# Kernel tuning notes

Measured on AMD Instinct MI355X. Metric: run time of the kernel, lower is better.

Reference implementation:

```python
import jax, jax.numpy as jnp
import numpy as np

N, FEAT, D, K, L, H, NCLS = 4096, 512, 64, 100, 3, 8, 2
EPS = 1e-15

def _ln(x, g, b, eps=1e-6):
    m = x.mean(-1, keepdims=True)
    v = x.var(-1, keepdims=True)
    return (x - m) * jax.lax.rsqrt(v + eps) * g + b


def setup_inputs():
    key = jax.random.key(0)
    ks = jax.random.split(key, 12)
    w = lambda k, shape: jax.random.normal(k, shape, jnp.float32) * 0.02
    return {
        "node_feat": jax.random.normal(ks[0], (1, N, FEAT), jnp.float32),
        "adj": jax.random.uniform(ks[1], (1, N, N), jnp.float32),
        "conv_w": w(ks[2], (FEAT, D)), "conv_b": jnp.zeros((D,), jnp.float32),
        "bn_g": jnp.ones((D,), jnp.float32), "bn_b": jnp.zeros((D,), jnp.float32),
        "pool_w": w(ks[3], (D, K)), "pool_b": jnp.zeros((K,), jnp.float32),
        "cls_token": jnp.zeros((1, 1, D), jnp.float32),
        "ln1_g": jnp.ones((L, D), jnp.float32), "ln1_b": jnp.zeros((L, D), jnp.float32),
        "qkv_w": w(ks[4], (L, D, 3 * D)), "qkv_b": jnp.zeros((L, 3 * D), jnp.float32),
        "proj_w": w(ks[5], (L, D, D)), "proj_b": jnp.zeros((L, D), jnp.float32),
        "ln2_g": jnp.ones((L, D), jnp.float32), "ln2_b": jnp.zeros((L, D), jnp.float32),
        "fc1_w": w(ks[6], (L, D, 4 * D)), "fc1_b": jnp.zeros((L, 4 * D), jnp.float32),
        "fc2_w": w(ks[7], (L, 4 * D, D)), "fc2_b": jnp.zeros((L, D), jnp.float32),
        "norm_g": jnp.ones((D,), jnp.float32), "norm_b": jnp.zeros((D,), jnp.float32),
        "head_w": w(ks[8], (D, NCLS)), "head_b": jnp.zeros((NCLS,), jnp.float32),
    }


def _forward(node_feat, adj, conv_w, conv_b, bn_g, bn_b, pool_w, pool_b, cls_token,
             ln1_g, ln1_b, qkv_w, qkv_b, proj_w, proj_b, ln2_g, ln2_b,
             fc1_w, fc1_b, fc2_w, fc2_b, norm_g, norm_b, head_w, head_b):
    x = node_feat  # mask is all ones -> X = mask*X is a no-op
    # --- GCNBlock: propagate + self loop + linear + BatchNorm(train stats) + L2 norm ---
    y = jnp.matmul(adj, x) + x                 # [1,N,F]
    y = y @ conv_w + conv_b                    # [1,N,D]
    m = y.mean(axis=(0, 1))
    v = y.var(axis=(0, 1))
    y = (y - m) * jax.lax.rsqrt(v + 1e-5) * bn_g + bn_b
    y = y / jnp.maximum(jnp.linalg.norm(y, axis=2, keepdims=True), 1e-12)
    # --- cluster assignment ---
    s = jax.nn.softmax(y @ pool_w + pool_b, axis=-1)   # [1,N,K]
    # --- dense_mincut_pool ---
    out = jnp.einsum('bnk,bnd->bkd', s, y)             # [1,K,D]
    sa = s[0].T @ adj[0]                               # [K,N] (the torch.sparse.mm)
    out_adj = (sa @ s[0])[None]                        # [1,K,K]
    mincut_num = jnp.trace(out_adj, axis1=1, axis2=2)  # [1]
    d_flat = adj.sum(-1)                               # [1,N] degrees
    # trace(S^T diag(d) S) = sum_i d_i * ||s_i||^2
    mincut_den = jnp.sum(d_flat[0] * jnp.sum(s[0] ** 2, axis=-1))[None]
    mincut_loss = jnp.mean(-(mincut_num / mincut_den))
    ss = jnp.einsum('bnk,bnl->bkl', s, s)
    i_s = jnp.eye(K, dtype=ss.dtype)
    ortho_loss = jnp.mean(jnp.linalg.norm(
        ss / jnp.linalg.norm(ss, axis=(-1, -2), keepdims=True) - i_s / jnp.linalg.norm(i_s),
        axis=(-1, -2)))
    ind = jnp.arange(K)
    out_adj = out_adj.at[:, ind, ind].set(0.0)
    dd = jnp.sqrt(out_adj.sum(-1))[:, None] + EPS      # [1,1,K]
    out_adj = out_adj / dd / jnp.swapaxes(dd, 1, 2)    # (returned by pool; unused downstream)
    # --- transformer over [cls] + K cluster tokens ---
    t = jnp.concatenate([jnp.broadcast_to(cls_token, (1, 1, D)), out], axis=1)  # [1,K+1,D]
    hd = D // H
    scale = hd ** -0.5
    for l in range(L):
        h = _ln(t, ln1_g[l], ln1_b[l])
        qkv = h @ qkv_w[l] + qkv_b[l]
        q, k, vv = jnp.split(qkv, 3, axis=-1)
        sp = lambda a: a.reshape(1, -1, H, hd).transpose(0, 2, 1, 3)
        q, k, vv = sp(q), sp(k), sp(vv)
        att = jax.nn.softmax(jnp.einsum('bhqd,bhkd->bhqk', q, k) * scale, axis=-1)
        o = jnp.einsum('bhqk,bhkd->bhqd', att, vv).transpose(0, 2, 1, 3).reshape(1, -1, D)
        t = t + (o @ proj_w[l] + proj_b[l])
        h = _ln(t, ln2_g[l], ln2_b[l])
        t = t + (jax.nn.gelu(h @ fc1_w[l] + fc1_b[l], approximate=False) @ fc2_w[l] + fc2_b[l])
    t = _ln(t, norm_g, norm_b)
    logits = t[:, 0] @ head_w + head_b                 # [1,NCLS]
    return logits, mincut_loss, ortho_loss


def reference(node_feat, adj, conv_w, conv_b, bn_g, bn_b, pool_w, pool_b, cls_token,
              ln1_g, ln1_b, qkv_w, qkv_b, proj_w, proj_b, ln2_g, ln2_b,
              fc1_w, fc1_b, fc2_w, fc2_b, norm_g, norm_b, head_w, head_b):
    return _forward(node_feat, adj, conv_w, conv_b, bn_g, bn_b, pool_w, pool_b, cls_token,
                    ln1_g, ln1_b, qkv_w, qkv_b, proj_w, proj_b, ln2_g, ln2_b,
                    fc1_w, fc1_b, fc2_w, fc2_b, norm_g, norm_b, head_w, head_b)
```

## Files before the change

kernel.cpp:

```cpp
#include <hip/hip_runtime.h>
#include <hip/hip_bf16.h>
#include <math.h>

#define NN   4096
#define FEAT 512
#define DIM  64
#define KC   100
#define LL   3

#define OFF_DFLAT   0
#define OFF_CHSUM   4096
#define OFF_CHSQ    4160
#define ZERO_FLOATS 4224
#define OFF_XW      4224
#define OFF_YPART   (OFF_XW + NN*DIM)
#define OFF_GPART   (OFF_YPART + 8*NN*DIM)
#define OFF_Y0      (OFF_GPART + 64*128*192)
#define OFF_TBUF    (OFF_Y0 + NN*DIM)
#define OFF_QKV     (OFF_TBUF + 101*DIM)
#define OFF_SS      (OFF_QKV + 101*192)
#define OFF_DENP    (OFF_SS + KC*KC)
#define OFF_NUMP    (OFF_DENP + 1024)
#define OFF_SB16    (OFF_NUMP + 1024)
#define OFF_STB16   (OFF_SB16 + NN*128/2)
#define OFF_YNT16   (OFF_STB16 + NN*128/2)
#define OFF_XWT16   (OFF_YNT16 + NN*DIM/2)

typedef __attribute__((ext_vector_type(8))) short bfrag;
typedef __attribute__((ext_vector_type(4))) float ffrag;

__device__ __forceinline__ unsigned short f2bf(float f) {
    union { float f; unsigned u; } v; v.f = f;
    return (unsigned short)((v.u + 0x7FFFu + ((v.u >> 16) & 1u)) >> 16);
}
__device__ __forceinline__ float bf2f(unsigned short u) {
    union { unsigned u; float f; } v; v.u = (unsigned)u << 16; return v.f;
}
__device__ __forceinline__ unsigned int pk2(float a, float b) {
    __hip_bfloat162 h = __float22bfloat162_rn(make_float2(a, b));
    return *(unsigned int*)&h;
}

__device__ __forceinline__ float wsum(float v) {
#pragma unroll
    for (int o = 32; o > 0; o >>= 1) v += __shfl_xor(v, o, 64);
    return v;
}
__device__ __forceinline__ float wmax(float v) {
#pragma unroll
    for (int o = 32; o > 0; o >>= 1) v = fmaxf(v, __shfl_xor(v, o, 64));
    return v;
}
__device__ __forceinline__ float hsum32(float v) {
#pragma unroll
    for (int o = 16; o > 0; o >>= 1) v += __shfl_xor(v, o, 64);
    return v;
}
__device__ __forceinline__ float hmax32(float v) {
#pragma unroll
    for (int o = 16; o > 0; o >>= 1) v = fmaxf(v, __shfl_xor(v, o, 64));
    return v;
}

__global__ __launch_bounds__(256) void xwk(const float* __restrict__ x,
                                           const float* __restrict__ B,
                                           float* __restrict__ xw,
                                           unsigned short* __restrict__ xwT,
                                           float* __restrict__ zws) {
    __shared__ float a_sh[16 * 68];
    __shared__ float b_sh[64 * 68];
    __shared__ unsigned short tl[64 * 17];
    const int t = threadIdx.x, rb = blockIdx.x;
    if (rb < 17) {
        const int zi = rb * 256 + t;
        if (zi < ZERO_FLOATS) zws[zi] = 0.f;
    }
    const int r = t >> 4, cg = (t & 15) * 4;
    float4 acc = make_float4(0.f, 0.f, 0.f, 0.f);
    for (int kt = 0; kt < FEAT; kt += 64) {
        *(float4*)&a_sh[(t >> 4) * 68 + (t & 15) * 4] =
            *(const float4*)(x + (size_t)(rb * 16 + (t >> 4)) * FEAT + kt + (t & 15) * 4);
#pragma unroll
        for (int p = 0; p < 4; ++p) {
            const int idx = t + 256 * p;
// ... 58 lines not shown
        }
        __syncthreads();
#pragma unroll
        for (int ks = 0; ks < 2; ++ks) {
            const bfrag af = *(const bfrag*)(a_sh + (ih * 16 + m) * 72 + ks * 32 + q * 8);
#pragma unroll
            for (int jj = 0; jj < 2; ++jj) {
                const bfrag bf = *(const bfrag*)(b_sh + ((jh * 2 + jj) * 16 + m) * 72 + ks * 32 + q * 8);
                acc[jj] = __builtin_amdgcn_mfma_f32_16x16x32_bf16(af, bf, acc[jj], 0, 0, 0);
            }
        }
        __syncthreads();
    }
    float* op = ypart + (size_t)blockIdx.y * NN * DIM;
#pragma unroll
    for (int jj = 0; jj < 2; ++jj)
#pragma unroll
        for (int r = 0; r < 4; ++r)
            op[(size_t)(rb * 32 + ih * 16 + q * 4 + r) * DIM + jh * 32 + jj * 16 + m] = acc[jj][r];
    dacc += __shfl_down(dacc, 1, 64);
    dacc += __shfl_down(dacc, 2, 64);
    dacc += __shfl_down(dacc, 4, 64);
    if (sq == 0) atomicAdd(&dflat[rb * 32 + srow], dacc);
}

__global__ __launch_bounds__(256) void spmmT(const float* __restrict__ adj,
                                             const unsigned short* __restrict__ ST,
                                             const unsigned short* __restrict__ Sb16,
                                             float* __restrict__ nump) {
    __shared__ __align__(16) unsigned short a_sh[32 * 72];
    __shared__ __align__(16) unsigned short s_sh[128 * 72];
    __shared__ float red[4];
    const int t  = threadIdx.x;
    const int rb = blockIdx.x;
    const int k0 = blockIdx.y * 512;
    const int w = t >> 6, lane = t & 63;
    const int m = lane & 15, q = lane >> 4;
    const int rh = w & 1, ch = w >> 1;
    const int srow = t >> 3, sq = t & 7;
    const int sn = t >> 1, sc2 = t & 1;
    ffrag acc[4];
#pragma unroll
    for (int j = 0; j < 4; ++j) acc[j] = (ffrag){0.f, 0.f, 0.f, 0.f};
    const float* abase = adj + (size_t)(rb * 32 + srow) * NN + k0;
    const unsigned short* sbase = ST + (size_t)sn * NN + k0;
    for (int kt = 0; kt < 512; kt += 64) {
#pragma unroll
        for (int k = 0; k < 2; ++k) {
            const int p = sq + 8 * k;
            const float4 v = *(const float4*)(abase + kt + 4 * p);
            *(uint2*)(a_sh + srow * 72 + 4 * p) = make_uint2(pk2(v.x, v.y), pk2(v.z, v.w));
        }
#pragma unroll
        for (int k = 0; k < 4; ++k) {
            const int c2 = sc2 + 2 * k;
            *(bfrag*)(s_sh + sn * 72 + c2 * 8) = *(const bfrag*)(sbase + kt + c2 * 8);
        }
        __syncthreads();
#pragma unroll
        for (int ks = 0; ks < 2; ++ks) {
            const bfrag af = *(const bfrag*)(a_sh + (rh * 16 + m) * 72 + ks * 32 + q * 8);
#pragma unroll
            for (int j = 0; j < 4; ++j) {
                const bfrag bf = *(const bfrag*)(s_sh + ((ch * 4 + j) * 16 + m) * 72 + ks * 32 + q * 8);
                acc[j] = __builtin_amdgcn_mfma_f32_16x16x32_bf16(af, bf, acc[j], 0, 0, 0);
            }
        }
        __syncthreads();
    }
    float local = 0.f;
#pragma unroll
    for (int j = 0; j < 4; ++j)
#pragma unroll
        for (int r = 0; r < 4; ++r) {
            const int row = rb * 32 + rh * 16 + q * 4 + r;
            const int col = ch * 64 + j * 16 + m;
            local += acc[j][r] * bf2f(Sb16[(size_t)row * 128 + col]);
        }
    local = wsum(local);
    if (lane == 0) red[w] = local;
    __syncthreads();
    if (t == 0) nump[blockIdx.y * 128 + blockIdx.x] = red[0] + red[1] + red[2] + red[3];
}

__global__ __launch_bounds__(256) void bnstat(const float* __restrict__ ypart,
                                              const float* __restrict__ xw,
                                              const float* __restrict__ conv_b,
                                              float* __restrict__ Y0,
                                              float* __restrict__ chsum,
                                              float* __restrict__ chsq) {
    __shared__ float ssum[64], ssq[64];
    const int t = threadIdx.x;
    if (t < 64) { ssum[t] = 0.f; ssq[t] = 0.f; }
    __syncthreads();
    const int tid = blockIdx.x * 256 + t;
    const size_t e = (size_t)tid * 4;
    const int c0 = (int)(e & 63);
    float4 v = *(const float4*)(xw + e);
#pragma unroll
    for (int s = 0; s < 8; ++s) {
        const float4 u = *(const float4*)(ypart + (size_t)s * NN * DIM + e);
        v.x += u.x; v.y += u.y; v.z += u.z; v.w += u.w;
    }
    const float4 b = *(const float4*)(conv_b + c0);
    v.x += b.x; v.y += b.y; v.z += b.z; v.w += b.w;
// ... 67 lines not shown
    Sb16[(size_t)row * 128 + lane] = b1;
    Sb16[(size_t)row * 128 + 64 + lane] = b2;
    sb_sh[w][lane] = b1;
    sb_sh[w][64 + lane] = b2;
    const float c = wsum(s1 * s1 + s2 * s2);
    if (lane == 0) denw[w] = dflat[row] * c;
    __syncthreads();
    if (t < 64) {
        ushort4 o;
        o.x = f2bf(yn_sh[0][t]); o.y = f2bf(yn_sh[1][t]);
        o.z = f2bf(yn_sh[2][t]); o.w = f2bf(yn_sh[3][t]);
        *(ushort4*)(YnT + (size_t)t * NN + blockIdx.x * 4) = o;
    } else if (t < 192) {
        const int c2 = t - 64;
        ushort4 o;
        o.x = sb_sh[0][c2]; o.y = sb_sh[1][c2];
        o.z = sb_sh[2][c2]; o.w = sb_sh[3][c2];
        *(ushort4*)(ST + (size_t)c2 * NN + blockIdx.x * 4) = o;
    } else if (t == 192) {
        denp[blockIdx.x] = denw[0] + denw[1] + denw[2] + denw[3];
    }
}

__global__ __launch_bounds__(256) void gram(const unsigned short* __restrict__ ST,
                                            const unsigned short* __restrict__ YnT,
                                            float* __restrict__ gpart) {
    __shared__ __align__(16) unsigned short a_sh[128 * 72];
    __shared__ __align__(16) unsigned short b_sh[192 * 72];
    const int t = threadIdx.x;
    const int k0 = blockIdx.x * 64;
    const int w = t >> 6, lane = t & 63;
    const int m = lane & 15, q = lane >> 4;
#pragma unroll
    for (int p = 0; p < 4; ++p) {
        const int n = (t >> 3) + 32 * p, c = t & 7;
        *(bfrag*)(a_sh + n * 72 + c * 8) = *(const bfrag*)(ST + (size_t)n * NN + k0 + c * 8);
    }
#pragma unroll
    for (int p = 0; p < 6; ++p) {
        const int n = (t >> 3) + 32 * p, c = t & 7;
        const unsigned short* src = (n < 64) ? (YnT + (size_t)n * NN + k0 + c * 8)
                                             : (ST + (size_t)(n - 64) * NN + k0 + c * 8);
        *(bfrag*)(b_sh + n * 72 + c * 8) = *(const bfrag*)src;
    }
    __syncthreads();
    ffrag acc[2][12];
#pragma unroll
    for (int i = 0; i < 2; ++i)
#pragma unroll
        for (int j = 0; j < 12; ++j) acc[i][j] = (ffrag){0.f, 0.f, 0.f, 0.f};
#pragma unroll
    for (int ks = 0; ks < 2; ++ks) {
        const bfrag af0 = *(const bfrag*)(a_sh + (w * 32 +  0 + m) * 72 + ks * 32 + q * 8);
        const bfrag af1 = *(const bfrag*)(a_sh + (w * 32 + 16 + m) * 72 + ks * 32 + q * 8);
#pragma unroll
        for (int j = 0; j < 12; ++j) {
            const bfrag bf = *(const bfrag*)(b_sh + (j * 16 + m) * 72 + ks * 32 + q * 8);
            acc[0][j] = __builtin_amdgcn_mfma_f32_16x16x32_bf16(af0, bf, acc[0][j], 0, 0, 0);
            acc[1][j] = __builtin_amdgcn_mfma_f32_16x16x32_bf16(af1, bf, acc[1][j], 0, 0, 0);
        }
    }
    float* op = gpart + (size_t)blockIdx.x * 128 * 192;
#pragma unroll
    for (int i = 0; i < 2; ++i)
#pragma unroll
        for (int j = 0; j < 12; ++j)
#pragma unroll
            for (int r = 0; r < 4; ++r)
                op[(size_t)(w * 32 + i * 16 + q * 4 + r) * 192 + j * 16 + m] = acc[i][j][r];
}

__global__ __launch_bounds__(256) void gramred(const float* __restrict__ gpart,
                                               const float* __restrict__ cls,
                                               float* __restrict__ tbuf,
                                               float* __restrict__ ss) {
    const int tid = blockIdx.x * 256 + threadIdx.x;
    if (tid < 128 * 192) {
        const int row = tid / 192, col = tid - row * 192;
        float v = 0.f;
        for (int s = 0; s < 64; ++s) v += gpart[(size_t)s * 128 * 192 + tid];
        if (row < KC) {
            if (col < 64) tbuf[(row + 1) * 64 + col] = v;
            else if (col < 164) ss[row * KC + (col - 64)] = v;
        }
    } else if (tid < 128 * 192 + 64) {
        const int c = tid - 128 * 192;
        tbuf[c] = cls[c];
    }
}

__global__ __launch_bounds__(512) void attnA(const float* __restrict__ tbuf,
                                             const float* __restrict__ g1,
                                             const float* __restrict__ b1,
                                             const float* __restrict__ qw,
                                             const float* __restrict__ qb,
                                             float* __restrict__ qkvb, int l) {
    __shared__ float wl[64 * 192];
    __shared__ float hs[64];
    __shared__ float part[2][196];
    const int t = threadIdx.x, tok = blockIdx.x;
    const float* wsrc = qw + (size_t)l * 64 * 192;
#pragma unroll
    for (int p = 0; p < 6; ++p) {
        const int idx = t + 512 * p;
        ((float4*)wl)[idx] = ((const float4*)wsrc)[idx];
    }
    if (t < 64) {
        const float x = tbuf[tok * 64 + t];
        const float m = wsum(x) * (1.f / 64.f);
        const float var = wsum(x * x) * (1.f / 64.f) - m * m;
        hs[t] = (x - m) * rsqrtf(var + 1e-6f) * g1[l * 64 + t] + b1[l * 64 + t];
    }
    __syncthreads();
    if (t < 384) {
        const int o = t % 192, grp = t / 192;
        float a = 0.f;
#pragma unroll 8
        for (int e = grp * 32; e < grp * 32 + 32; ++e)
            a += hs[e] * wl[e * 192 + o];
        part[grp][o] = a;
    }
    __syncthreads();
    if (t < 192)
        qkvb[tok * 192 + t] = qb[l * 192 + t] + part[0][t] + part[1][t];
}

__global__ __launch_bounds__(512) void attnB(float* __restrict__ tbuf,
                                             float* __restrict__ qkvb,
                                             const float* __restrict__ pw,
                                             const float* __restrict__ pb,
                                             const float* __restrict__ g2,
                                             const float* __restrict__ b2,
                                             const float* __restrict__ w1,
                                             const float* __restrict__ bb1,
                                             const float* __restrict__ w2,
                                             const float* __restrict__ bb2,
                                             const float* __restrict__ g1,
                                             const float* __restrict__ b1,
                                             const float* __restrict__ qw,
                                             const float* __restrict__ qb,
                                             int l) {
    __shared__ float big[13332];
    __shared__ float sc[8 * 104];
    __shared__ float part[8][132];
    __shared__ float q_l[64], osh[64], h2sh[64], gsh[256];
    __shared__ float h1sh[64];
    float* part2 = (float*)part;
    const int t = threadIdx.x, qtok = blockIdx.x;
    float t_old = 0.f;
    if (t < 64) t_old = tbuf[qtok * 64 + t];
#pragma unroll
    for (int p = 0; p < 7; ++p) {
        const int idx = t + 512 * p;
        if (idx < 101 * 32) {
            const int k = idx >> 5, c = idx & 31;
            *(float4*)&big[k * 132 + c * 4] = *(const float4*)(qkvb + k * 192 + 64 + c * 4);
        }
    }
    if (t < 16) *(float4*)&q_l[t * 4] = *(const float4*)(qkvb + qtok * 192 + t * 4);
    __syncthreads();
    const float scale = 0.35355339059327373f;
#pragma unroll
    for (int p = 0; p < 2; ++p) {
        const int idx = t + 512 * p;
        if (idx < 808) {
            const int h = idx / 101, k = idx - h * 101;
            float s = 0.f;
#pragma unroll
            for (int d = 0; d < 8; ++d)
                s += q_l[h * 8 + d] * big[k * 132 + h * 8 + d];
            sc[h * 104 + k] = s * scale;
        }
    }
    __syncthreads();
    if (t < 256) {
        const int w = t >> 6;
        const int h = w * 2 + ((t >> 5) & 1);
        const int lft = t & 31;
        float v[4];
#pragma unroll
        for (int g = 0; g < 4; ++g) {
            const int k = lft + 32 * g;
            v[g] = (k < 101) ? sc[h * 104 + k] : -1e30f;
        }
        float m = fmaxf(fmaxf(v[0], v[1]), fmaxf(v[2], v[3]));
        m = hmax32(m);
        float s = 0.f;
#pragma unroll
        for (int g = 0; g < 4; ++g) { v[g] = expf(v[g] - m); s += v[g]; }
        s = hsum32(s);
        const float inv = 1.f / s;
#pragma unroll
        for (int g = 0; g < 4; ++g) {
            const int k = lft + 32 * g;
            if (k < 101) sc[h * 104 + k] = v[g] * inv;
        }
    }
    __syncthreads();
    {
        const int o = t & 63, grp = t >> 6;
        float po = 0.f;
        for (int k = grp; k < 101; k += 8)
            po += sc[(o >> 3) * 104 + k] * big[k * 132 + 64 + o];
        part[grp][o] = po;
    }
    __syncthreads();
    if (t < 64)
        osh[t] = part[0][t] + part[1][t] + part[2][t] + part[3][t]
               + part[4][t] + part[5][t] + part[6][t] + part[7][t];
    __syncthreads();
#pragma unroll
    for (int p = 0; p < 2; ++p) {
        const int idx = t + 512 * p;
        ((float4*)big)[idx] = ((const float4*)(pw + (size_t)l * 4096))[idx];
    }
    __syncthreads();
    {
        const int o = t & 63, grp = t >> 6;
        float pp = 0.f;
#pragma unroll
        for (int e = grp * 8; e < grp * 8 + 8; ++e)
            pp += osh[e] * big[e * 64 + o];
        part[grp][o] = pp;
    }
    __syncthreads();
    float t1 = 0.f;
    if (t < 64) {
        float pr = pb[l * 64 + t];
#pragma unroll
        for (int g = 0; g < 8; ++g) pr += part[g][t];
        t1 = t_old + pr;
        const float m = wsum(t1) * (1.f / 64.f);
        const float var = wsum(t1 * t1) * (1.f / 64.f) - m * m;
        h2sh[t] = (t1 - m) * rsqrtf(var + 1e-6f) * g2[l * 64 + t] + b2[l * 64 + t];
    }
    __syncthreads();
    for (int ch = 0; ch < 2; ++ch) {
#pragma unroll
        for (int p = 0; p < 4; ++p) {
            const int idx = t + 512 * p;
            const int e = idx >> 5, c = idx & 31;
            *(float4*)&big[e * 128 + c * 4] =
                *(const float4*)(w1 + (size_t)l * 16384 + e * 256 + ch * 128 + c * 4);
        }
        __syncthreads();
        {
            const int o = t & 127, grp = t >> 7;
            float pa = 0.f;
#pragma unroll
            for (int e = grp * 16; e < grp * 16 + 16; ++e)
                pa += h2sh[e] * big[e * 128 + o];
            part[grp][o] = pa;
        }
        __syncthreads();
        if (t < 128) {
            float a = bb1[l * 256 + ch * 128 + t]
                    + part[0][t] + part[1][t] + part[2][t] + part[3][t];
            gsh[ch * 128 + t] = 0.5f * a * (1.f + erff(a * 0.70710678118654752f));
        }
        __syncthreads();
    }
    float a2p = 0.f;
    for (int ch = 0; ch < 2; ++ch) {
#pragma unroll
        for (int p = 0; p < 4; ++p) {
            const int idx = t + 512 * p;
            ((float4*)big)[idx] = ((const float4*)(w2 + (size_t)l * 16384 + ch * 8192))[idx];
        }
        __syncthreads();
        {
            const int o = t & 63, grp = t >> 6;
#pragma unroll
            for (int er = grp * 16; er < grp * 16 + 16; ++er)
                a2p += gsh[ch * 128 + er] * big[er * 64 + o];
        }
        __syncthreads();
    }
    {
        const int o = t & 63, grp = t >> 6;
        part[grp][o] = a2p;
    }
    __syncthreads();
    if (t < 64) {
        float a2 = bb2[l * 64 + t];
#pragma unroll
        for (int g = 0; g < 8; ++g) a2 += part[g][t];
        const float tn = t1 + a2;
        tbuf[qtok * 64 + t] = tn;
        if (l < 2) {
            const float m = wsum(tn) * (1.f / 64.f);
            const float var = wsum(tn * tn) * (1.f / 64.f) - m * m;
            h1sh[t] = (tn - m) * rsqrtf(var + 1e-6f) * g1[(l + 1) * 64 + t]
                      + b1[(l + 1) * 64 + t];
        }
    }
    if (l < 2) {
        __syncthreads();
#pragma unroll
        for (int p = 0; p < 6; ++p) {
            const int idx = t + 512 * p;
            ((float4*)big)[idx] = ((const float4*)(qw + (size_t)(l + 1) * 12288))[idx];
        }
        __syncthreads();
        if (t < 384) {
            const int o = t % 192, grp = t / 192;
            float a = 0.f;
#pragma unroll 8
            for (int e = grp * 32; e < grp * 32 + 32; ++e)
                a += h1sh[e] * big[e * 192 + o];
            part2[grp * 192 + o] = a;
        }
        __syncthreads();
        if (t < 192)
            qkvb[qtok * 192 + t] = qb[(l + 1) * 192 + t] + part2[t] + part2[192 + t];
    }
}

__global__ __launch_bounds__(256) void finalk(const float* __restrict__ tbuf,
                                              const float* __restrict__ ng,
                                              const float* __restrict__ nb,
                                              const float* __restrict__ hw,
                                              const float* __restrict__ hb,
                                              const float* __restrict__ ss,
                                              const float* __restrict__ denp,
                                              const float* __restrict__ nump,
                                              float* __restrict__ out) {
    __shared__ float f0[64];
    __shared__ float red[256];
    __shared__ float fro_sh, den_sh, num_sh;
    const int t = threadIdx.x;
    if (t < 64) {
        const float x = tbuf[t];
        const float m = wsum(x) * (1.f / 64.f);
        const float var = wsum(x * x) * (1.f / 64.f) - m * m;
        f0[t] = (x - m) * rsqrtf(var + 1e-6f) * ng[t] + nb[t];
    }
    red[t] = denp[t] + denp[t + 256] + denp[t + 512] + denp[t + 768];
    __syncthreads();
    for (int s = 128; s > 0; s >>= 1) { if (t < s) red[t] += red[t + s]; __syncthreads(); }
    if (t == 0) den_sh = red[0];
    __syncthreads();
    red[t] = nump[t] + nump[t + 256] + nump[t + 512] + nump[t + 768];
    __syncthreads();
    for (int s = 128; s > 0; s >>= 1) { if (t < s) red[t] += red[t + s]; __syncthreads(); }
    if (t == 0) num_sh = red[0];
    __syncthreads();
    if (t < 2) {
        float a = hb[t];
        for (int d = 0; d < 64; ++d) a += f0[d] * hw[d * 2 + t];
        out[t] = a;
    }
    if (t == 2) out[2] = -(num_sh / den_sh);
    float s1 = 0.f;
    for (int idx = t; idx < KC * KC; idx += 256) { const float v = ss[idx]; s1 += v * v; }
    __syncthreads();
    red[t] = s1;
    __syncthreads();
    for (int s = 128; s > 0; s >>= 1) { if (t < s) red[t] += red[t + s]; __syncthreads(); }
    if (t == 0) fro_sh = sqrtf(red[0]);
    __syncthreads();
    const float inv = 1.f / fro_sh;
    float s2 = 0.f;
    for (int idx = t; idx < KC * KC; idx += 256) {
        float v = ss[idx] * inv;
        if (idx % 101 == 0) v -= 0.1f;
        s2 += v * v;
    }
    __syncthreads();
    red[t] = s2;
    __syncthreads();
    for (int s = 128; s > 0; s >>= 1) { if (t < s) red[t] += red[t + s]; __syncthreads(); }
    if (t == 0) out[3] = sqrtf(red[0]);
}

extern "C" void kernel_launch(void* const* d_in, const int* in_sizes, int n_in,
                              void* d_out, int out_size, void* d_ws, size_t ws_size,
                              hipStream_t stream) {
    (void)in_sizes; (void)n_in; (void)out_size; (void)ws_size;
    const float* x      = (const float*)d_in[0];
    const float* adj    = (const float*)d_in[1];
    const float* conv_w = (const float*)d_in[2];
    const float* conv_b = (const float*)d_in[3];
    const float* bn_g   = (const float*)d_in[4];
    const float* bn_b   = (const float*)d_in[5];
    const float* pool_w = (const float*)d_in[6];
    const float* pool_b = (const float*)d_in[7];
    const float* cls    = (const float*)d_in[8];
    const float* ln1_g  = (const float*)d_in[9];
    const float* ln1_b  = (const float*)d_in[10];
    const float* qkv_w  = (const float*)d_in[11];
    const float* qkv_b  = (const float*)d_in[12];
    const float* proj_w = (const float*)d_in[13];
    const float* proj_b = (const float*)d_in[14];
    const float* ln2_g  = (const float*)d_in[15];
    const float* ln2_b  = (const float*)d_in[16];
    const float* fc1_w  = (const float*)d_in[17];
    const float* fc1_b  = (const float*)d_in[18];
    const float* fc2_w  = (const float*)d_in[19];
    const float* fc2_b  = (const float*)d_in[20];
    const float* norm_g = (const float*)d_in[21];
    const float* norm_b = (const float*)d_in[22];
    const float* head_w = (const float*)d_in[23];
    const float* head_b = (const float*)d_in[24];
    float* ws  = (float*)d_ws;
    float* out = (float*)d_out;
    unsigned short* Sb16  = (unsigned short*)(ws + OFF_SB16);
    unsigned short* STb16 = (unsigned short*)(ws + OFF_STB16);
    unsigned short* YnT16 = (unsigned short*)(ws + OFF_YNT16);
    unsigned short* xwT16 = (unsigned short*)(ws + OFF_XWT16);

    xwk<<<256, 256, 0, stream>>>(x, conv_w, ws + OFF_XW, xwT16, ws);
    gemmA<<<dim3(128, 8), 256, 0, stream>>>(adj, xwT16, ws + OFF_YPART, ws + OFF_DFLAT);
    bnstat<<<256, 256, 0, stream>>>(ws + OFF_YPART, ws + OFF_XW, conv_b,
                                    ws + OFF_Y0, ws + OFF_CHSUM, ws + OFF_CHSQ);
    rowsk<<<1024, 256, 0, stream>>>(ws + OFF_Y0, bn_g, bn_b, ws + OFF_CHSUM, ws + OFF_CHSQ,
                                    pool_w, pool_b, ws + OFF_DFLAT,
                                    YnT16, Sb16, STb16, ws + OFF_DENP);
    spmmT<<<dim3(128, 8), 256, 0, stream>>>(adj, STb16, Sb16, ws + OFF_NUMP);
    gram<<<64, 256, 0, stream>>>(STb16, YnT16, ws + OFF_GPART);
    gramred<<<97, 256, 0, stream>>>(ws + OFF_GPART, cls, ws + OFF_TBUF, ws + OFF_SS);
    attnA<<<101, 512, 0, stream>>>(ws + OFF_TBUF, ln1_g, ln1_b, qkv_w, qkv_b, ws + OFF_QKV, 0);
    for (int l = 0; l < LL; ++l) {
        attnB<<<101, 512, 0, stream>>>(ws + OFF_TBUF, ws + OFF_QKV, proj_w, proj_b,
                                       ln2_g, ln2_b, fc1_w, fc1_b, fc2_w, fc2_b,
                                       ln1_g, ln1_b, qkv_w, qkv_b, l);
    }
    finalk<<<1, 256, 0, stream>>>(ws + OFF_TBUF, norm_g, norm_b, head_w, head_b,
                                  ws + OFF_SS, ws + OFF_DENP, ws + OFF_NUMP, out);
}
```

Baseline: 284.8 us.

## Fuse spmm, gram, reduction, transformer layers and final into one persistent kernel

Replaces the spmmT, gram, gramred, attnA, the per-layer attnB and finalk launches with a single 256-block persistent kernel. Blocks beyond the 101 token blocks do the spmm and gram work, and the token blocks then run all transformer layers, synchronised through global atomic counters and spin-wait barriers. The aim is to remove launch overhead and inter-kernel gaps and to let the adjacency spmm overlap with the serial transformer chain. The cost is a dependence on all blocks being co-resident, since spin barriers can deadlock otherwise, plus extra atomic polling traffic.

```diff
diff --git a/kernel.cpp b/kernel.cpp
--- a/kernel.cpp
+++ b/kernel.cpp
@@ -11,13 +11,13 @@
 #define OFF_DFLAT   0
 #define OFF_CHSUM   4096
 #define OFF_CHSQ    4160
-#define ZERO_FLOATS 4224
-#define OFF_XW      4224
+#define OFF_CTR     4224
+#define ZERO_FLOATS 4240
+#define OFF_XW      4240
 #define OFF_YPART   (OFF_XW + NN*DIM)
 #define OFF_GPART   (OFF_YPART + 8*NN*DIM)
 #define OFF_Y0      (OFF_GPART + 64*128*192)
-#define OFF_TBUF    (OFF_Y0 + NN*DIM)
-#define OFF_QKV     (OFF_TBUF + 101*DIM)
+#define OFF_QKV     (OFF_Y0 + NN*DIM)
 #define OFF_SS      (OFF_QKV + 101*192)
 #define OFF_DENP    (OFF_SS + KC*KC)
 #define OFF_NUMP    (OFF_DENP + 1024)
@@ -60,6 +60,22 @@
 #pragma unroll
     for (int o = 16; o > 0; o >>= 1) v = fmaxf(v, __shfl_xor(v, o, 64));
     return v;
+}
+
+__device__ __forceinline__ unsigned acq_load(const unsigned* p) {
+    return __hip_atomic_load(p, __ATOMIC_ACQUIRE, __HIP_MEMORY_SCOPE_AGENT);
+}
+__device__ __forceinline__ void rel_add(unsigned* p) {
+    __hip_atomic_fetch_add(p, 1u, __ATOMIC_RELEASE, __HIP_MEMORY_SCOPE_AGENT);
+}
+__device__ __forceinline__ void gbar(unsigned* c, unsigned tgt) {
+    __threadfence();
+    __syncthreads();
+    if (threadIdx.x == 0) {
+        rel_add(c);
+        while (acq_load(c) < tgt) __builtin_amdgcn_s_sleep(2);
+    }
+    __syncthreads();
 }
 
 __global__ __launch_bounds__(256) void xwk(const float* __restrict__ x,
@@ -164,65 +180,6 @@
     dacc += __shfl_down(dacc, 2, 64);
     dacc += __shfl_down(dacc, 4, 64);
     if (sq == 0) atomicAdd(&dflat[rb * 32 + srow], dacc);
-}
-
-__global__ __launch_bounds__(256) void spmmT(const float* __restrict__ adj,
-                                             const unsigned short* __restrict__ ST,
-                                             const unsigned short* __restrict__ Sb16,
-                                             float* __restrict__ nump) {
-    __shared__ __align__(16) unsigned short a_sh[32 * 72];
-    __shared__ __align__(16) unsigned short s_sh[128 * 72];
-    __shared__ float red[4];
-    const int t  = threadIdx.x;
-    const int rb = blockIdx.x;
-    const int k0 = blockIdx.y * 512;
-    const int w = t >> 6, lane = t & 63;
-    const int m = lane & 15, q = lane >> 4;
-    const int rh = w & 1, ch = w >> 1;
-    const int srow = t >> 3, sq = t & 7;
-    const int sn = t >> 1, sc2 = t & 1;
-    ffrag acc[4];
-#pragma unroll
-    for (int j = 0; j < 4; ++j) acc[j] = (ffrag){0.f, 0.f, 0.f, 0.f};
-    const float* abase = adj + (size_t)(rb * 32 + srow) * NN + k0;
-    const unsigned short* sbase = ST + (size_t)sn * NN + k0;
-    for (int kt = 0; kt < 512; kt += 64) {
-#pragma unroll
-        for (int k = 0; k < 2; ++k) {
-            const int p = sq + 8 * k;
-            const float4 v = *(const float4*)(abase + kt + 4 * p);
-            *(uint2*)(a_sh + srow * 72 + 4 * p) = make_uint2(pk2(v.x, v.y), pk2(v.z, v.w));
-        }
-#pragma unroll
-        for (int k = 0; k < 4; ++k) {
-            const int c2 = sc2 + 2 * k;
-            *(bfrag*)(s_sh + sn * 72 + c2 * 8) = *(const bfrag*)(sbase + kt + c2 * 8);
-        }
-        __syncthreads();
-#pragma unroll
-        for (int ks = 0; ks < 2; ++ks) {
-            const bfrag af = *(const bfrag*)(a_sh + (rh * 16 + m) * 72 + ks * 32 + q * 8);
-#pragma unroll
-            for (int j = 0; j < 4; ++j) {
-                const bfrag bf = *(const bfrag*)(s_sh + ((ch * 4 + j) * 16 + m) * 72 + ks * 32 + q * 8);
-                acc[j] = __builtin_amdgcn_mfma_f32_16x16x32_bf16(af, bf, acc[j], 0, 0, 0);
-            }
-        }
-        __syncthreads();
-    }
-    float local = 0.f;
-#pragma unroll
-    for (int j = 0; j < 4; ++j)
-#pragma unroll
-        for (int r = 0; r < 4; ++r) {
-            const int row = rb * 32 + rh * 16 + q * 4 + r;
-            const int col = ch * 64 + j * 16 + m;
-            local += acc[j][r] * bf2f(Sb16[(size_t)row * 128 + col]);
-        }
-    local = wsum(local);
-    if (lane == 0) red[w] = local;
-    __syncthreads();
-    if (t == 0) nump[blockIdx.y * 128 + blockIdx.x] = red[0] + red[1] + red[2] + red[3];
 }
 
 __global__ __launch_bounds__(256) void bnstat(const float* __restrict__ ypart,
@@ -336,355 +293,381 @@
     }
 }
 
-__global__ __launch_bounds__(256) void gram(const unsigned short* __restrict__ ST,
-                                            const unsigned short* __restrict__ YnT,
-                                            float* __restrict__ gpart) {
-    __shared__ __align__(16) unsigned short a_sh[128 * 72];
-    __shared__ __align__(16) unsigned short b_sh[192 * 72];
-    const int t = threadIdx.x;
-    const int k0 = blockIdx.x * 64;
-    const int w = t >> 6, lane = t & 63;
-    const int m = lane & 15, q = lane >> 4;
-#pragma unroll
-    for (int p = 0; p < 4; ++p) {
-        const int n = (t >> 3) + 32 * p, c = t & 7;
-        *(bfrag*)(a_sh + n * 72 + c * 8) = *(const bfrag*)(ST + (size_t)n * NN + k0 + c * 8);
-    }
-#pragma unroll
-    for (int p = 0; p < 6; ++p) {
-        const int n = (t >> 3) + 32 * p, c = t & 7;
-        const unsigned short* src = (n < 64) ? (YnT + (size_t)n * NN + k0 + c * 8)
-                                             : (ST + (size_t)(n - 64) * NN + k0 + c * 8);
-        *(bfrag*)(b_sh + n * 72 + c * 8) = *(const bfrag*)src;
-    }
-    __syncthreads();
-    ffrag acc[2][12];
-#pragma unroll
-    for (int i = 0; i < 2; ++i)
-#pragma unroll
-        for (int j = 0; j < 12; ++j) acc[i][j] = (ffrag){0.f, 0.f, 0.f, 0.f};
-#pragma unroll
-    for (int ks = 0; ks < 2; ++ks) {
-        const bfrag af0 = *(const bfrag*)(a_sh + (w * 32 +  0 + m) * 72 + ks * 32 + q * 8);
-        const bfrag af1 = *(const bfrag*)(a_sh + (w * 32 + 16 + m) * 72 + ks * 32 + q * 8);
-#pragma unroll
-        for (int j = 0; j < 12; ++j) {
-            const bfrag bf = *(const bfrag*)(b_sh + (j * 16 + m) * 72 + ks * 32 + q * 8);
-            acc[0][j] = __builtin_amdgcn_mfma_f32_16x16x32_bf16(af0, bf, acc[0][j], 0, 0, 0);
-            acc[1][j] = __builtin_amdgcn_mfma_f32_16x16x32_bf16(af1, bf, acc[1][j], 0, 0, 0);
-        }
-    }
-    float* op = gpart + (size_t)blockIdx.x * 128 * 192;
-#pragma unroll
-    for (int i = 0; i < 2; ++i)
-#pragma unroll
-        for (int j = 0; j < 12; ++j)
-#pragma unroll
-            for (int r = 0; r < 4; ++r)
-                op[(size_t)(w * 32 + i * 16 + q * 4 + r) * 192 + j * 16 + m] = acc[i][j][r];
-}
-
-__global__ __launch_bounds__(256) void gramred(const float* __restrict__ gpart,
-                                               const float* __restrict__ cls,
-                                               float* __restrict__ tbuf,
-                                               float* __restrict__ ss) {
-    const int tid = blockIdx.x * 256 + threadIdx.x;
-    if (tid < 128 * 192) {
-        const int row = tid / 192, col = tid - row * 192;
-        float v = 0.f;
-        for (int s = 0; s < 64; ++s) v += gpart[(size_t)s * 128 * 192 + tid];
-        if (row < KC) {
-            if (col < 64) tbuf[(row + 1) * 64 + col] = v;
-            else if (col < 164) ss[row * KC + (col - 64)] = v;
-        }
-    } else if (tid < 128 * 192 + 64) {
-        const int c = tid - 128 * 192;
-        tbuf[c] = cls[c];
-    }
-}
-
-__global__ __launch_bounds__(512) void attnA(const float* __restrict__ tbuf,
-                                             const float* __restrict__ g1,
-                                             const float* __restrict__ b1,
-                                             const float* __restrict__ qw,
-                                             const float* __restrict__ qb,
-                                             float* __restrict__ qkvb, int l) {
-    __shared__ float wl[64 * 192];
-    __shared__ float hs[64];
-    __shared__ float part[2][196];
-    const int t = threadIdx.x, tok = blockIdx.x;
-    const float* wsrc = qw + (size_t)l * 64 * 192;
-#pragma unroll
-    for (int p = 0; p < 6; ++p) {
-        const int idx = t + 512 * p;
-        ((float4*)wl)[idx] = ((const float4*)wsrc)[idx];
-    }
-    if (t < 64) {
-        const float x = tbuf[tok * 64 + t];
-        const float m = wsum(x) * (1.f / 64.f);
-        const float var = wsum(x * x) * (1.f / 64.f) - m * m;
-        hs[t] = (x - m) * rsqrtf(var + 1e-6f) * g1[l * 64 + t] + b1[l * 64 + t];
-    }
-    __syncthreads();
-    if (t < 384) {
-        const int o = t % 192, grp = t / 192;
-        float a = 0.f;
+__global__ __launch_bounds__(512) void xform(
+        const float* __restrict__ adj,
+        const unsigned short* __restrict__ ST,
+        const unsigned short* __restrict__ Sb16,
+        const unsigned short* __restrict__ YnT,
+        float* __restrict__ gpart,
+        const float* __restrict__ cls,
+        float* __restrict__ ssb,
+        float* __restrict__ qkvb,
+        const float* __restrict__ g1, const float* __restrict__ b1,
+        const float* __restrict__ qw, const float* __restrict__ qb,
+        const float* __restrict__ pw, const float* __restrict__ pb,
+        const float* __restrict__ g2, const float* __restrict__ b2,
+        const float* __restrict__ w1, const float* __restrict__ bb1,
+        const float* __restrict__ w2, const float* __restrict__ bb2,
+        const float* __restrict__ ng, const float* __restrict__ nb,
+        const float* __restrict__ hw, const float* __restrict__ hb,
+        const float* __restrict__ denp, float* __restrict__ nump,
+        unsigned* __restrict__ ctr,
+        float* __restrict__ out) {
+    __shared__ __align__(16) float big[13332];
+    __shared__ float scsh[8 * 104];
+    __shared__ __align__(16) float partf[1056];
+    __shared__ float q_l[64], osh[64], h2sh[64], h1sh[64], toksh[64], gsh[256];
+    __shared__ float redw8[8];
+    float (*part)[132] = (float(*)[132])partf;
+    const int t = threadIdx.x, b = blockIdx.x;
+
+    if (b < 101) {
+        if (b == 0) {
+            if (t < 64) toksh[t] = cls[t];
+        } else {
+            if (t == 0) { while (acq_load(&ctr[3]) < 64u) __builtin_amdgcn_s_sleep(2); }
+            __syncthreads();
+            const int row = b - 1;
+            if (t < 384) {
+                const int col = t % 192, sg = t / 192;
+                float v = 0.f;
+                const float* gp = gpart + (size_t)row * 192 + col + (size_t)sg * 32 * 24576;
+                for (int s = 0; s < 32; ++s) v += gp[(size_t)s * 24576];
+                partf[sg * 192 + col] = v;
+            }
+            __syncthreads();
+            if (t < 192) {
+                const float v = partf[t] + partf[192 + t];
+                if (t < 64) toksh[t] = v;
+                else if (t < 164) ssb[row * 100 + (t - 64)] = v;
+            }
+        }
+        __syncthreads();
+        if (t < 64) {
+            const float x = toksh[t];
+            const float m = wsum(x) * (1.f / 64.f);
+            const float var = wsum(x * x) * (1.f / 64.f) - m * m;
+            h1sh[t] = (x - m) * rsqrtf(var + 1e-6f) * g1[t] + b1[t];
+        }
+        __syncthreads();
+        for (int l = 0; l < LL; ++l) {
+#pragma unroll
+            for (int p = 0; p < 6; ++p) {
+                const int idx = t + 512 * p;
+                ((float4*)big)[idx] = ((const float4*)(qw + (size_t)l * 12288))[idx];
+            }
+            __syncthreads();
+            if (t < 384) {
+                const int o = t % 192, grp = t / 192;
+                float a = 0.f;
 #pragma unroll 8
-        for (int e = grp * 32; e < grp * 32 + 32; ++e)
-            a += hs[e] * wl[e * 192 + o];
-        part[grp][o] = a;
-    }
-    __syncthreads();
-    if (t < 192)
-        qkvb[tok * 192 + t] = qb[l * 192 + t] + part[0][t] + part[1][t];
-}
-
-__global__ __launch_bounds__(512) void attnB(float* __restrict__ tbuf,
-                                             float* __restrict__ qkvb,
-                                             const float* __restrict__ pw,
-                                             const float* __restrict__ pb,
-                                             const float* __restrict__ g2,
-                                             const float* __restrict__ b2,
-                                             const float* __restrict__ w1,
-                                             const float* __restrict__ bb1,
-                                             const float* __restrict__ w2,
-                                             const float* __restrict__ bb2,
-                                             const float* __restrict__ g1,
-                                             const float* __restrict__ b1,
-                                             const float* __restrict__ qw,
-                                             const float* __restrict__ qb,
-                                             int l) {
-    __shared__ float big[13332];
-    __shared__ float sc[8 * 104];
-    __shared__ float part[8][132];
-    __shared__ float q_l[64], osh[64], h2sh[64], gsh[256];
-    __shared__ float h1sh[64];
-    float* part2 = (float*)part;
-    const int t = threadIdx.x, qtok = blockIdx.x;
-    float t_old = 0.f;
-    if (t < 64) t_old = tbuf[qtok * 64 + t];
-#pragma unroll
-    for (int p = 0; p < 7; ++p) {
-        const int idx = t + 512 * p;
-        if (idx < 101 * 32) {
-            const int k = idx >> 5, c = idx & 31;
-            *(float4*)&big[k * 132 + c * 4] = *(const float4*)(qkvb + k * 192 + 64 + c * 4);
-        }
-    }
-    if (t < 16) *(float4*)&q_l[t * 4] = *(const float4*)(qkvb + qtok * 192 + t * 4);
-    __syncthreads();
-    const float scale = 0.35355339059327373f;
-#pragma unroll
-    for (int p = 0; p < 2; ++p) {
-        const int idx = t + 512 * p;
-        if (idx < 808) {
-            const int h = idx / 101, k = idx - h * 101;
-            float s = 0.f;
-#pragma unroll
-            for (int d = 0; d < 8; ++d)
-                s += q_l[h * 8 + d] * big[k * 132 + h * 8 + d];
-            sc[h * 104 + k] = s * scale;
-        }
-    }
-    __syncthreads();
-    if (t < 256) {
-        const int w = t >> 6;
-        const int h = w * 2 + ((t >> 5) & 1);
-        const int lft = t & 31;
-        float v[4];
-#pragma unroll
-        for (int g = 0; g < 4; ++g) {
-            const int k = lft + 32 * g;
-            v[g] = (k < 101) ? sc[h * 104 + k] : -1e30f;
-        }
-        float m = fmaxf(fmaxf(v[0], v[1]), fmaxf(v[2], v[3]));
-        m = hmax32(m);
-        float s = 0.f;
-#pragma unroll
-        for (int g = 0; g < 4; ++g) { v[g] = expf(v[g] - m); s += v[g]; }
-        s = hsum32(s);
-        const float inv = 1.f / s;
-#pragma unroll
-        for (int g = 0; g < 4; ++g) {
-            const int k = lft + 32 * g;
-            if (k < 101) sc[h * 104 + k] = v[g] * inv;
-        }
-    }
-    __syncthreads();
-    {
-        const int o = t & 63, grp = t >> 6;
-        float po = 0.f;
-        for (int k = grp; k < 101; k += 8)
-            po += sc[(o >> 3) * 104 + k] * big[k * 132 + 64 + o];
-        part[grp][o] = po;
-    }
-    __syncthreads();
-    if (t < 64)
-        osh[t] = part[0][t] + part[1][t] + part[2][t] + part[3][t]
-               + part[4][t] + part[5][t] + part[6][t] + part[7][t];
-    __syncthreads();
-#pragma unroll
-    for (int p = 0; p < 2; ++p) {
-        const int idx = t + 512 * p;
-        ((float4*)big)[idx] = ((const float4*)(pw + (size_t)l * 4096))[idx];
-    }
-    __syncthreads();
-    {
-        const int o = t & 63, grp = t >> 6;
-        float pp = 0.f;
-#pragma unroll
-        for (int e = grp * 8; e < grp * 8 + 8; ++e)
-            pp += osh[e] * big[e * 64 + o];
-        part[grp][o] = pp;
-    }
-    __syncthreads();
-    float t1 = 0.f;
-    if (t < 64) {
-        float pr = pb[l * 64 + t];
-#pragma unroll
-        for (int g = 0; g < 8; ++g) pr += part[g][t];
-        t1 = t_old + pr;
-        const float m = wsum(t1) * (1.f / 64.f);
-        const float var = wsum(t1 * t1) * (1.f / 64.f) - m * m;
-        h2sh[t] = (t1 - m) * rsqrtf(var + 1e-6f) * g2[l * 64 + t] + b2[l * 64 + t];
-    }
-    __syncthreads();
-    for (int ch = 0; ch < 2; ++ch) {
-#pragma unroll
-        for (int p = 0; p < 4; ++p) {
-            const int idx = t + 512 * p;
-            const int e = idx >> 5, c = idx & 31;
-            *(float4*)&big[e * 128 + c * 4] =
-                *(const float4*)(w1 + (size_t)l * 16384 + e * 256 + ch * 128 + c * 4);
-        }
+                for (int e = grp * 32; e < grp * 32 + 32; ++e)
+                    a += h1sh[e] * big[e * 192 + o];
+                partf[grp * 192 + o] = a;
+            }
+            __syncthreads();
+            if (t < 192)
+                qkvb[b * 192 + t] = qb[l * 192 + t] + partf[t] + partf[192 + t];
+            gbar(&ctr[l], 101u);
+            float t_old = 0.f;
+            if (t < 64) t_old = toksh[t];
+#pragma unroll
+            for (int p = 0; p < 7; ++p) {
+                const int idx = t + 512 * p;
+                if (idx < 101 * 32) {
+                    const int k = idx >> 5, c = idx & 31;
+                    *(float4*)&big[k * 132 + c * 4] = *(const float4*)(qkvb + k * 192 + 64 + c * 4);
+                }
+            }
+            if (t < 16) *(float4*)&q_l[t * 4] = *(const float4*)(qkvb + b * 192 + t * 4);
+            __syncthreads();
+            const float scale = 0.35355339059327373f;
+#pragma unroll
+            for (int p = 0; p < 2; ++p) {
+                const int idx = t + 512 * p;
+                if (idx < 808) {
+                    const int h = idx / 101, k = idx - h * 101;
+                    float s = 0.f;
+#pragma unroll
+                    for (int d = 0; d < 8; ++d)
+                        s += q_l[h * 8 + d] * big[k * 132 + h * 8 + d];
+                    scsh[h * 104 + k] = s * scale;
+                }
+            }
+            __syncthreads();
+            if (t < 256) {
+                const int w = t >> 6;
+                const int h = w * 2 + ((t >> 5) & 1);
+                const int lft = t & 31;
+                float v[4];
+#pragma unroll
+                for (int g = 0; g < 4; ++g) {
+                    const int k = lft + 32 * g;
+                    v[g] = (k < 101) ? scsh[h * 104 + k] : -1e30f;
+                }
+                float mm = fmaxf(fmaxf(v[0], v[1]), fmaxf(v[2], v[3]));
+                mm = hmax32(mm);
+                float s = 0.f;
+#pragma unroll
+                for (int g = 0; g < 4; ++g) { v[g] = expf(v[g] - mm); s += v[g]; }
+                s = hsum32(s);
+                const float inv = 1.f / s;
+#pragma unroll
+                for (int g = 0; g < 4; ++g) {
+                    const int k = lft + 32 * g;
+                    if (k < 101) scsh[h * 104 + k] = v[g] * inv;
+                }
+            }
+            __syncthreads();
+            {
+                const int o = t & 63, grp = t >> 6;
+                float po = 0.f;
+                for (int k = grp; k < 101; k += 8)
+                    po += scsh[(o >> 3) * 104 + k] * big[k * 132 + 64 + o];
+                part[grp][o] = po;
+            }
+            __syncthreads();
+            if (t < 64)
+                osh[t] = part[0][t] + part[1][t] + part[2][t] + part[3][t]
+                       + part[4][t] + part[5][t] + part[6][t] + part[7][t];
+            __syncthreads();
+#pragma unroll
+            for (int p = 0; p < 2; ++p) {
+                const int idx = t + 512 * p;
+                ((float4*)big)[idx] = ((const float4*)(pw + (size_t)l * 4096))[idx];
+            }
+            __syncthreads();
+            {
+                const int o = t & 63, grp = t >> 6;
+                float pp = 0.f;
+#pragma unroll
+                for (int e = grp * 8; e < grp * 8 + 8; ++e)
+                    pp += osh[e] * big[e * 64 + o];
+                part[grp][o] = pp;
+            }
+            __syncthreads();
+            float t1 = 0.f;
+            if (t < 64) {
+                float pr = pb[l * 64 + t];
+#pragma unroll
+                for (int g = 0; g < 8; ++g) pr += part[g][t];
+                t1 = t_old + pr;
+                const float m = wsum(t1) * (1.f / 64.f);
+                const float var = wsum(t1 * t1) * (1.f / 64.f) - m * m;
+                h2sh[t] = (t1 - m) * rsqrtf(var + 1e-6f) * g2[l * 64 + t] + b2[l * 64 + t];
+            }
+            __syncthreads();
+            for (int ch = 0; ch < 2; ++ch) {
+#pragma unroll
+                for (int p = 0; p < 4; ++p) {
+                    const int idx = t + 512 * p;
+                    const int e = idx >> 5, c = idx & 31;
+                    *(float4*)&big[e * 128 + c * 4] =
+                        *(const float4*)(w1 + (size_t)l * 16384 + e * 256 + ch * 128 + c * 4);
+                }
+                __syncthreads();
+                {
+                    const int o = t & 127, grp = t >> 7;
+                    float pa = 0.f;
+#pragma unroll
+                    for (int e = grp * 16; e < grp * 16 + 16; ++e)
+                        pa += h2sh[e] * big[e * 128 + o];
+                    part[grp][o] = pa;
+                }
+                __syncthreads();
+                if (t < 128) {
+                    float a = bb1[l * 256 + ch * 128 + t]
+                            + part[0][t] + part[1][t] + part[2][t] + part[3][t];
+                    gsh[ch * 128 + t] = 0.5f * a * (1.f + erff(a * 0.70710678118654752f));
+                }
+                __syncthreads();
+            }
+            float a2p = 0.f;
+            for (int ch = 0; ch < 2; ++ch) {
+#pragma unroll
+                for (int p = 0; p < 4; ++p) {
+                    const int idx = t + 512 * p;
+                    ((float4*)big)[idx] = ((const float4*)(w2 + (size_t)l * 16384 + ch * 8192))[idx];
+                }
+                __syncthreads();
+                {
+                    const int o = t & 63, grp = t >> 6;
+#pragma unroll
+                    for (int er = grp * 16; er < grp * 16 + 16; ++er)
+                        a2p += gsh[ch * 128 + er] * big[er * 64 + o];
+                }
+                __syncthreads();
+            }
+            {
+                const int o = t & 63, grp = t >> 6;
+                part[grp][o] = a2p;
+            }
+            __syncthreads();
+            if (t < 64) {
+                float a2 = bb2[l * 64 + t];
+#pragma unroll
+                for (int g = 0; g < 8; ++g) a2 += part[g][t];
+                const float tn = t1 + a2;
+                toksh[t] = tn;
+                if (l < 2) {
+                    const float m = wsum(tn) * (1.f / 64.f);
+                    const float var = wsum(tn * tn) * (1.f / 64.f) - m * m;
+                    h1sh[t] = (tn - m) * rsqrtf(var + 1e-6f) * g1[(l + 1) * 64 + t]
+                              + b1[(l + 1) * 64 + t];
+                }
+            }
+            __syncthreads();
+        }
+        if (b == 0) {
+            if (t < 64) {
+                const float x = toksh[t];
+                const float m = wsum(x) * (1.f / 64.f);
+                const float var = wsum(x * x) * (1.f / 64.f) - m * m;
+                h1sh[t] = (x - m) * rsqrtf(var + 1e-6f) * ng[t] + nb[t];
+            }
+            if (t == 0) { while (acq_load(&ctr[4]) < 155u) __builtin_amdgcn_s_sleep(8); }
+            __syncthreads();
+            float* red = partf;
+            red[t] = denp[t] + denp[t + 512];
+            __syncthreads();
+            for (int s = 256; s > 0; s >>= 1) { if (t < s) red[t] += red[t + s]; __syncthreads(); }
+            if (t == 0) q_l[0] = red[0];
+            __syncthreads();
+            red[t] = nump[t] + nump[t + 512];
+            __syncthreads();
+            for (int s = 256; s > 0; s >>= 1) { if (t < s) red[t] += red[t + s]; __syncthreads(); }
+            if (t == 0) q_l[1] = red[0];
+            __syncthreads();
+            if (t < 2) {
+                float a = hb[t];
+                for (int d = 0; d < 64; ++d) a += h1sh[d] * hw[d * 2 + t];
+                out[t] = a;
+            }
+            if (t == 2) out[2] = -(q_l[1] / q_l[0]);
+            float s1 = 0.f;
+            for (int idx = t; idx < KC * KC; idx += 512) { const float v = ssb[idx]; s1 += v * v; }
+            __syncthreads();
+            red[t] = s1;
+            __syncthreads();
+            for (int s = 256; s > 0; s >>= 1) { if (t < s) red[t] += red[t + s]; __syncthreads(); }
+            if (t == 0) q_l[2] = sqrtf(red[0]);
+            __syncthreads();
+            const float inv = 1.f / q_l[2];
+            float s2 = 0.f;
+            for (int idx = t; idx < KC * KC; idx += 512) {
+                float v = ssb[idx] * inv;
+                if (idx % 101 == 0) v -= 0.1f;
+                s2 += v * v;
+            }
+            __syncthreads();
+            red[t] = s2;
+            __syncthreads();
+            for (int s = 256; s > 0; s >>= 1) { if (t < s) red[t] += red[t + s]; __syncthreads(); }
+            if (t == 0) out[3] = sqrtf(red[0]);
+        }
+    } else {
+        const int wb = b - 101;
+        const int w = t >> 6, lane = t & 63;
+        const int m = lane & 15, q = lane >> 4;
+        if (wb < 64) {
+            unsigned short* a_sh = (unsigned short*)big;
+            unsigned short* b_sh = (unsigned short*)big + 128 * 72;
+            const int k0 = wb * 64;
+            const int n0 = t >> 3, c8 = (t & 7) * 8;
+#pragma unroll
+            for (int p = 0; p < 2; ++p) {
+                const int n = n0 + 64 * p;
+                *(bfrag*)(a_sh + n * 72 + c8) = *(const bfrag*)(ST + (size_t)n * NN + k0 + c8);
+            }
+#pragma unroll
+            for (int p = 0; p < 3; ++p) {
+                const int n = n0 + 64 * p;
+                const unsigned short* src = (n < 64) ? (YnT + (size_t)n * NN + k0 + c8)
+                                                     : (ST + (size_t)(n - 64) * NN + k0 + c8);
+                *(bfrag*)(b_sh + n * 72 + c8) = *(const bfrag*)src;
+            }
+            __syncthreads();
+            ffrag acc[12];
+#pragma unroll
+            for (int j = 0; j < 12; ++j) acc[j] = (ffrag){0.f, 0.f, 0.f, 0.f};
+#pragma unroll
+            for (int ks = 0; ks < 2; ++ks) {
+                const bfrag af = *(const bfrag*)(a_sh + (w * 16 + m) * 72 + ks * 32 + q * 8);
+#pragma unroll
+                for (int j = 0; j < 12; ++j) {
+                    const bfrag bf = *(const bfrag*)(b_sh + (j * 16 + m) * 72 + ks * 32 + q * 8);
+                    acc[j] = __builtin_amdgcn_mfma_f32_16x16x32_bf16(af, bf, acc[j], 0, 0, 0);
+                }
+            }
+            float* op = gpart + (size_t)wb * 128 * 192;
+#pragma unroll
+            for (int j = 0; j < 12; ++j)
+#pragma unroll
+                for (int r = 0; r < 4; ++r)
+                    op[(size_t)(w * 16 + q * 4 + r) * 192 + j * 16 + m] = acc[j][r];
+            __threadfence();
+            __syncthreads();
+            if (t == 0) rel_add(&ctr[3]);
+        }
+        unsigned short* a_sh = (unsigned short*)big;
+        unsigned short* s_sh = (unsigned short*)big + 32 * 72;
+        const int rh = w & 1, ch = w >> 1;
+        const int srow = t >> 4, sq4 = (t & 15) * 4;
+        const int sn = t >> 2, scq = t & 3;
+        for (int tile = wb; tile < 1024; tile += 155) {
+            const int rb = tile & 127;
+            const int k0 = (tile >> 7) * 512;
+            ffrag acc[2];
+            acc[0] = (ffrag){0.f, 0.f, 0.f, 0.f};
+            acc[1] = (ffrag){0.f, 0.f, 0.f, 0.f};
+            const float* abase = adj + (size_t)(rb * 32 + srow) * NN + k0;
+            const unsigned short* sbase = ST + (size_t)sn * NN + k0;
+            for (int kt = 0; kt < 512; kt += 64) {
+                {
+                    const float4 v = *(const float4*)(abase + kt + sq4);
+                    *(uint2*)(a_sh + srow * 72 + sq4) = make_uint2(pk2(v.x, v.y), pk2(v.z, v.w));
+                }
+#pragma unroll
+                for (int k = 0; k < 2; ++k) {
+                    const int c2 = scq + 4 * k;
+                    *(bfrag*)(s_sh + sn * 72 + c2 * 8) = *(const bfrag*)(sbase + kt + c2 * 8);
+                }
+                __syncthreads();
+#pragma unroll
+                for (int ks = 0; ks < 2; ++ks) {
+                    const bfrag af = *(const bfrag*)(a_sh + (rh * 16 + m) * 72 + ks * 32 + q * 8);
+#pragma unroll
+                    for (int j = 0; j < 2; ++j) {
+                        const bfrag bf = *(const bfrag*)(s_sh + ((ch * 2 + j) * 16 + m) * 72 + ks * 32 + q * 8);
+                        acc[j] = __builtin_amdgcn_mfma_f32_16x16x32_bf16(af, bf, acc[j], 0, 0, 0);
+                    }
+                }
+                __syncthreads();
+            }
+            float local = 0.f;
+#pragma unroll
+            for (int j = 0; j < 2; ++j)
+#pragma unroll
+                for (int r = 0; r < 4; ++r) {
+                    const int row = rb * 32 + rh * 16 + q * 4 + r;
+                    const int col = ch * 32 + j * 16 + m;
+                    local += acc[j][r] * bf2f(Sb16[(size_t)row * 128 + col]);
+                }
+            local = wsum(local);
+            if (lane == 0) redw8[w] = local;
+            __syncthreads();
+            if (t == 0) {
+                float s = 0.f;
+#pragma unroll
+                for (int k = 0; k < 8; ++k) s += redw8[k];
+                nump[(tile >> 7) * 128 + rb] = s;
+            }
+            __syncthreads();
+        }
+        __threadfence();
         __syncthreads();
-        {
-            const int o = t & 127, grp = t >> 7;
-            float pa = 0.f;
-#pragma unroll
-            for (int e = grp * 16; e < grp * 16 + 16; ++e)
-                pa += h2sh[e] * big[e * 128 + o];
-            part[grp][o] = pa;
-        }
-        __syncthreads();
-        if (t < 128) {
-            float a = bb1[l * 256 + ch * 128 + t]
-                    + part[0][t] + part[1][t] + part[2][t] + part[3][t];
-            gsh[ch * 128 + t] = 0.5f * a * (1.f + erff(a * 0.70710678118654752f));
-        }
-        __syncthreads();
-    }
-    float a2p = 0.f;
-    for (int ch = 0; ch < 2; ++ch) {
-#pragma unroll
-        for (int p = 0; p < 4; ++p) {
-            const int idx = t + 512 * p;
-            ((float4*)big)[idx] = ((const float4*)(w2 + (size_t)l * 16384 + ch * 8192))[idx];
-        }
-        __syncthreads();
-        {
-            const int o = t & 63, grp = t >> 6;
-#pragma unroll
-            for (int er = grp * 16; er < grp * 16 + 16; ++er)
-                a2p += gsh[ch * 128 + er] * big[er * 64 + o];
-        }
-        __syncthreads();
-    }
-    {
-        const int o = t & 63, grp = t >> 6;
-        part[grp][o] = a2p;
-    }
-    __syncthreads();
-    if (t < 64) {
-        float a2 = bb2[l * 64 + t];
-#pragma unroll
-        for (int g = 0; g < 8; ++g) a2 += part[g][t];
-        const float tn = t1 + a2;
-        tbuf[qtok * 64 + t] = tn;
-        if (l < 2) {
-            const float m = wsum(tn) * (1.f / 64.f);
-            const float var = wsum(tn * tn) * (1.f / 64.f) - m * m;
-            h1sh[t] = (tn - m) * rsqrtf(var + 1e-6f) * g1[(l + 1) * 64 + t]
-                      + b1[(l + 1) * 64 + t];
-        }
-    }
-    if (l < 2) {
-        __syncthreads();
-#pragma unroll
-        for (int p = 0; p < 6; ++p) {
-            const int idx = t + 512 * p;
-            ((float4*)big)[idx] = ((const float4*)(qw + (size_t)(l + 1) * 12288))[idx];
-        }
-        __syncthreads();
-        if (t < 384) {
-            const int o = t % 192, grp = t / 192;
-            float a = 0.f;
-#pragma unroll 8
-            for (int e = grp * 32; e < grp * 32 + 32; ++e)
-                a += h1sh[e] * big[e * 192 + o];
-            part2[grp * 192 + o] = a;
-        }
-        __syncthreads();
-        if (t < 192)
-            qkvb[qtok * 192 + t] = qb[(l + 1) * 192 + t] + part2[t] + part2[192 + t];
-    }
-}
-
-__global__ __launch_bounds__(256) void finalk(const float* __restrict__ tbuf,
-                                              const float* __restrict__ ng,
-                                              const float* __restrict__ nb,
-                                              const float* __restrict__ hw,
-                                              const float* __restrict__ hb,
-                                              const float* __restrict__ ss,
-                                              const float* __restrict__ denp,
-                                              const float* __restrict__ nump,
-                                              float* __restrict__ out) {
-    __shared__ float f0[64];
-    __shared__ float red[256];
-    __shared__ float fro_sh, den_sh, num_sh;
-    const int t = threadIdx.x;
-    if (t < 64) {
-        const float x = tbuf[t];
-        const float m = wsum(x) * (1.f / 64.f);
-        const float var = wsum(x * x) * (1.f / 64.f) - m * m;
-        f0[t] = (x - m) * rsqrtf(var + 1e-6f) * ng[t] + nb[t];
-    }
-    red[t] = denp[t] + denp[t + 256] + denp[t + 512] + denp[t + 768];
-    __syncthreads();
-    for (int s = 128; s > 0; s >>= 1) { if (t < s) red[t] += red[t + s]; __syncthreads(); }
-    if (t == 0) den_sh = red[0];
-    __syncthreads();
-    red[t] = nump[t] + nump[t + 256] + nump[t + 512] + nump[t + 768];
-    __syncthreads();
-    for (int s = 128; s > 0; s >>= 1) { if (t < s) red[t] += red[t + s]; __syncthreads(); }
-    if (t == 0) num_sh = red[0];
-    __syncthreads();
-    if (t < 2) {
-        float a = hb[t];
-        for (int d = 0; d < 64; ++d) a += f0[d] * hw[d * 2 + t];
-        out[t] = a;
-    }
-    if (t == 2) out[2] = -(num_sh / den_sh);
-    float s1 = 0.f;
-    for (int idx = t; idx < KC * KC; idx += 256) { const float v = ss[idx]; s1 += v * v; }
-    __syncthreads();
-    red[t] = s1;
-    __syncthreads();
-    for (int s = 128; s > 0; s >>= 1) { if (t < s) red[t] += red[t + s]; __syncthreads(); }
-    if (t == 0) fro_sh = sqrtf(red[0]);
-    __syncthreads();
-    const float inv = 1.f / fro_sh;
-    float s2 = 0.f;
-    for (int idx = t; idx < KC * KC; idx += 256) {
-        float v = ss[idx] * inv;
-        if (idx % 101 == 0) v -= 0.1f;
-        s2 += v * v;
-    }
-    __syncthreads();
-    red[t] = s2;
-    __syncthreads();
-    for (int s = 128; s > 0; s >>= 1) { if (t < s) red[t] += red[t + s]; __syncthreads(); }
-    if (t == 0) out[3] = sqrtf(red[0]);
+        if (t == 0) rel_add(&ctr[4]);
+    }
 }
 
 extern "C" void kernel_launch(void* const* d_in, const int* in_sizes, int n_in,
@@ -730,15 +713,11 @@
     rowsk<<<1024, 256, 0, stream>>>(ws + OFF_Y0, bn_g, bn_b, ws + OFF_CHSUM, ws + OFF_CHSQ,
                                     pool_w, pool_b, ws + OFF_DFLAT,
                                     YnT16, Sb16, STb16, ws + OFF_DENP);
-    spmmT<<<dim3(128, 8), 256, 0, stream>>>(adj, STb16, Sb16, ws + OFF_NUMP);
-    gram<<<64, 256, 0, stream>>>(STb16, YnT16, ws + OFF_GPART);
-    gramred<<<97, 256, 0, stream>>>(ws + OFF_GPART, cls, ws + OFF_TBUF, ws + OFF_SS);
-    attnA<<<101, 512, 0, stream>>>(ws + OFF_TBUF, ln1_g, ln1_b, qkv_w, qkv_b, ws + OFF_QKV, 0);
-    for (int l = 0; l < LL; ++l) {
-        attnB<<<101, 512, 0, stream>>>(ws + OFF_TBUF, ws + OFF_QKV, proj_w, proj_b,
-                                       ln2_g, ln2_b, fc1_w, fc1_b, fc2_w, fc2_b,
-                                       ln1_g, ln1_b, qkv_w, qkv_b, l);
-    }
-    finalk<<<1, 256, 0, stream>>>(ws + OFF_TBUF, norm_g, norm_b, head_w, head_b,
-                                  ws + OFF_SS, ws + OFF_DENP, ws + OFF_NUMP, out);
-}
+    xform<<<256, 512, 0, stream>>>(adj, STb16, Sb16, YnT16, ws + OFF_GPART, cls,
+                                   ws + OFF_SS, ws + OFF_QKV,
+                                   ln1_g, ln1_b, qkv_w, qkv_b, proj_w, proj_b,
+                                   ln2_g, ln2_b, fc1_w, fc1_b, fc2_w, fc2_b,
+                                   norm_g, norm_b, head_w, head_b,
+                                   ws + OFF_DENP, ws + OFF_NUMP,
+                                   (unsigned*)(ws + OFF_CTR), out);
+}
```

Result: slower. 390.6 us (+37.1%).
